# Performance work log

Hardware: AMD Instinct MI355X
Metric: run time of the kernel (lower is better)

## Reference

```python
import math
import jax, jax.numpy as jnp
import numpy as np

D_MODEL = 1024
N_HEAD = 16
D_HEAD = 64
Q_LEN = 2048
MEM_LEN = 2048
K_LEN = MEM_LEN + Q_LEN
B = 1
LN_EPS = 1e-5


def setup_inputs() -> dict:
    key = jax.random.key(0)
    ks = jax.random.split(key, 8)
    hidden = jax.random.normal(ks[0], (B, Q_LEN, D_MODEL), dtype=jnp.float32)
    position_embedding = jax.random.normal(ks[1], (K_LEN, D_MODEL), dtype=jnp.float32)
    u = jax.random.normal(ks[2], (N_HEAD, D_HEAD), dtype=jnp.float32) * 0.02
    v = jax.random.normal(ks[3], (N_HEAD, D_HEAD), dtype=jnp.float32) * 0.02
    memory = jax.random.normal(ks[4], (B, MEM_LEN, D_MODEL), dtype=jnp.float32)
    # TXL causal mask: query i may attend to key j iff j <= i + MEM_LEN
    i = jnp.arange(Q_LEN)[:, None]
    j = jnp.arange(K_LEN)[None, :]
    mask = (j > (i + MEM_LEN))[None, None]  # (1,1,Q,K) bool, True = masked
    # weights (torch Linear has no bias here); stored as (in, out)
    s = 1.0 / math.sqrt(D_MODEL)
    W_qkv = jax.random.normal(ks[5], (D_MODEL, 3 * N_HEAD * D_HEAD), dtype=jnp.float32) * s
    W_pe = jax.random.normal(ks[6], (D_MODEL, N_HEAD * D_HEAD), dtype=jnp.float32) * s
    W_out = jax.random.normal(ks[7], (N_HEAD * D_HEAD, D_MODEL), dtype=jnp.float32) * (1.0 / math.sqrt(N_HEAD * D_HEAD))
    return {"hidden": hidden, "position_embedding": position_embedding, "u": u,
            "v": v, "mask": mask, "memory": memory,
            "W_qkv": W_qkv, "W_pe": W_pe, "W_out": W_out}


def _layer_norm(x):
    # elementwise_affine=False LayerNorm over last dim
    mu = jnp.mean(x, axis=-1, keepdims=True)
    var = jnp.var(x, axis=-1, keepdims=True)
    return (x - mu) / jnp.sqrt(var + LN_EPS)


def reference(hidden, position_embedding, u, v, mask, memory, W_qkv, W_pe, W_out):
    batch, q_len, _ = hidden.shape
    k_len = position_embedding.shape[0]
    scale = 1.0 / math.sqrt(D_HEAD)

    mh = jnp.concatenate([memory, hidden], axis=1)          # (B, k_len, d_model)
    qkv = mh @ W_qkv                                        # post-norm: no LN on input
    Q, K, V = jnp.split(qkv, 3, axis=-1)
    Q = Q[:, -q_len:, :]
    pe = position_embedding @ W_pe                          # (k_len, H*D)

    Q = Q.reshape(batch, q_len, N_HEAD, D_HEAD)
    K = K.reshape(batch, k_len, N_HEAD, D_HEAD)
    V = V.reshape(batch, k_len, N_HEAD, D_HEAD)
    pe = pe.reshape(batch, k_len, N_HEAD, D_HEAD)

    AC = jnp.einsum('bqhd,bkhd->bhqk', Q + u, K)
    BD = jnp.einsum('bqhd,bkhd->bhqk', Q + v, pe)
    # NOTE: the original module calls relative_shift(BD) but DISCARDS the
    # result, so BD is used unshifted. We faithfully reproduce that.
    score = (AC + BD) * scale
    score = jnp.where(mask, -jnp.inf, score)
    prob = jax.nn.softmax(score, axis=-1)                   # (B,H,Q,K)
    av = jnp.einsum('bhqk,bkhd->bqhd', prob, V)
    av = av.reshape(batch, q_len, N_HEAD * D_HEAD)
    attn_out = av @ W_out
    return _layer_norm(hidden + attn_out)                   # post-norm residual
```

## Files before the change

kernel.cpp:

```cpp
#include <hip/hip_runtime.h>

typedef __attribute__((ext_vector_type(4))) float f32x4;
typedef __attribute__((ext_vector_type(16))) float f32x16;
typedef __attribute__((ext_vector_type(8))) short bf16x8;
typedef __attribute__((ext_vector_type(4))) unsigned short u16x4;
typedef unsigned short u16;

#define DM 1024
#define NHEAD 16
#define DHEAD 64
#define QLEN 2048
#define MLEN 2048
#define KLEN 4096
#define QSCALE 0.18033688011112042f

__device__ __forceinline__ float bf2f(u16 u) {
    unsigned i = ((unsigned)u) << 16; float f; __builtin_memcpy(&f, &i, 4); return f;
}
__device__ __forceinline__ u16 f2bf(float f) {
    unsigned i; __builtin_memcpy(&i, &f, 4);
    unsigned r = i + 0x7fffu + ((i >> 16) & 1u);
    return (u16)(r >> 16);
}
__device__ __forceinline__ float exp2_fast(float x) {
#if __has_builtin(__builtin_amdgcn_exp2f)
    return __builtin_amdgcn_exp2f(x);
#else
    return exp2f(x);
#endif
}
__device__ __forceinline__ unsigned cvtpk_bf16(float lo, float hi) {
    unsigned r;
    asm("v_cvt_pk_bf16_f32 %0, %1, %2" : "=v"(r) : "v"(lo), "v"(hi));
    return r;
}
__device__ __forceinline__ void gl2lds16(const void* g, void* l) {
    __builtin_amdgcn_global_load_lds((const __attribute__((address_space(1))) void*)g,
                                     (__attribute__((address_space(3))) void*)l, 16, 0, 0);
}

__global__ __launch_bounds__(256) void prep(
    const float* __restrict__ memory, const float* __restrict__ hidden,
    const float* __restrict__ pos, const float* __restrict__ Wqkv,
    const float* __restrict__ Wpe, const float* __restrict__ Wout,
    u16* __restrict__ MH, u16* __restrict__ PEA,
    u16* __restrict__ WQKVT, u16* __restrict__ WPET, u16* __restrict__ WOUTT)
{
    __shared__ float ls[64][65];
    const int b = blockIdx.x, t = threadIdx.x;
    if (b < 8192) {
        size_t e = ((size_t)b * 256 + t) * 4;
        const size_t HALF = (size_t)KLEN * DM;
        f32x4 v; u16* dst;
        if (e < HALF) {
            size_t row = e >> 10, col = e & 1023;
            const float* src = (row < MLEN) ? (memory + row * DM) : (hidden + (row - MLEN) * DM);
            v = *(const f32x4*)(src + col);
            dst = MH + e;
        } else {
            size_t e2 = e - HALF;
            v = *(const f32x4*)(pos + e2);
            dst = PEA + e2;
        }
        u16x4 o;
        #pragma unroll
        for (int c = 0; c < 4; ++c) o[c] = f2bf(v[c]);
        *(u16x4*)dst = o;
        return;
    }
    int tb = b - 8192;
    const float* src; u16* dst; int N, bx, by;
    if (tb < 768)       { src = Wqkv; dst = WQKVT; N = 3 * DM; bx = tb % 48; by = tb / 48; }
    else if (tb < 1024) { int i = tb - 768;  src = Wpe;  dst = WPET;  N = DM; bx = i & 15; by = i >> 4; }
    else                { int i = tb - 1024; src = Wout; dst = WOUTT; N = DM; bx = i & 15; by = i >> 4; }
    const int n0 = bx * 64, k0 = by * 64;
    const int c = t & 63, rg = t >> 6;
    #pragma unroll
    for (int p = 0; p < 16; ++p) {
        int r = p * 4 + rg;
        ls[r][c] = src[(size_t)(k0 + r) * N + n0 + c];
    }
    __syncthreads();
    #pragma unroll
    for (int p = 0; p < 16; ++p) {
        int r = p * 4 + rg;
        dst[(size_t)(n0 + r) * DM + k0 + c] = f2bf(ls[c][r]);
    }
}

__global__ __launch_bounds__(256, 3) void gemm_qkvpe(
    const u16* __restrict__ MH, const u16* __restrict__ PEA,
    const u16* __restrict__ WQKVT, const u16* __restrict__ WPET,
    const float* __restrict__ u, const float* __restrict__ vv,
    u16* __restrict__ QHAT, u16* __restrict__ KHAT, u16* __restrict__ VB)
{
    __shared__ u16 lsA[128 * 64];
    __shared__ u16 lsB[128 * 64];
    const int b = blockIdx.x;
    int row0, col0, region; const u16 *A, *B;
    if (b < 512)      { row0 = (b >> 4) * 128; col0 = 1024 + (b & 15) * 128; A = MH; B = WQKVT;
                        region = (col0 < 2048) ? 1 : 2; }
    else if (b < 640) { int i = b - 512; row0 = 2048 + (i >> 3) * 128; col0 = (i & 7) * 128;
                        A = MH; B = WQKVT; region = 0; }
    else              { int i = b - 640; row0 = (i >> 3) * 128; col0 = (i & 7) * 128;
                        A = PEA; B = WPET; region = 3; }
    const int tid = threadIdx.x, wave = tid >> 6, lane = tid & 63;
    const int blk = lane >> 4, ln = lane & 15;
    const int wr = (wave >> 1) << 6, wc = (wave & 1) << 6;
    const int rstage = lane >> 3;
    const int cstage = (lane & 7) * 8;

    f32x4 acc[4][4];
    #pragma unroll
    for (int i = 0; i < 4; ++i)
        #pragma unroll
        for (int j = 0; j < 4; ++j) acc[i][j] = f32x4{0.f, 0.f, 0.f, 0.f};

    for (int k0 = 0; k0 < DM; k0 += 64) {
        #pragma unroll
        for (int t = 0; t < 4; ++t) {
            int chunk = wave * 4 + t;
            int r = chunk * 8 + rstage;
            gl2lds16(A + (size_t)(row0 + r) * DM + k0 + cstage, lsA + chunk * 512);
            gl2lds16(B + (size_t)(col0 + r) * DM + k0 + cstage, lsB + chunk * 512);
        }
        __syncthreads();
        #pragma unroll
        for (int kk = 0; kk < 2; ++kk) {
            bf16x8 af[4], bfr[4];
            #pragma unroll
            for (int i = 0; i < 4; ++i)
                af[i] = *(const bf16x8*)(lsA + (wr + i * 16 + ln) * 64 + kk * 32 + blk * 8);
            #pragma unroll
            for (int j = 0; j < 4; ++j)
                bfr[j] = *(const bf16x8*)(lsB + (wc + j * 16 + ln) * 64 + kk * 32 + blk * 8);
            #pragma unroll
            for (int i = 0; i < 4; ++i)
                #pragma unroll
                for (int j = 0; j < 4; ++j)
                    acc[i][j] = __builtin_amdgcn_mfma_f32_16x16x32_bf16(af[i], bfr[j], acc[i][j], 0, 0, 0);
        }
        __syncthreads();
    }
    #pragma unroll
    for (int i = 0; i < 4; ++i)
        #pragma unroll
        for (int j = 0; j < 4; ++j)
            #pragma unroll
            for (int r = 0; r < 4; ++r) {
                int row = row0 + wr + i * 16 + blk * 4 + r;
                int col = col0 + wc + j * 16 + ln;
                float val = acc[i][j][r];
                if (region == 0) {
                    int q = row - MLEN, h = col >> 6;
                    size_t base = ((size_t)h * QLEN + q) * 128 + (col & 63);
                    QHAT[base]      = f2bf((val + u[col]) * QSCALE);
                    QHAT[base + 64] = f2bf((val + vv[col]) * QSCALE);
                } else if (region == 1) {
                    int c = col - 1024, h = c >> 6;
                    KHAT[((size_t)h * KLEN + row) * 128 + (c & 63)] = f2bf(val);
                } else if (region == 2) {
                    VB[(size_t)row * DM + (col - 2048)] = f2bf(val);
                } else {
                    int h = col >> 6;
                    KHAT[((size_t)h * KLEN + row) * 128 + 64 + (col & 63)] = f2bf(val);
                }
            }
}

__global__ __launch_bounds__(256) void pack_vt(const u16* __restrict__ VB, u16* __restrict__ VT)
{
    __shared__ float ls[64][65];
    const int kt = blockIdx.x, h = blockIdx.y;
    const int t = threadIdx.x, c = t & 63, rg = t >> 6;
    #pragma unroll
    for (int p = 0; p < 16; ++p) {
        int r = p * 4 + rg;
        ls[r][c] = bf2f(VB[(size_t)(kt * 64 + r) * DM + h * 64 + c]);
    }
    __syncthreads();
    #pragma unroll
    for (int p = 0; p < 16; ++p) {
        int d = p * 4 + rg;
        VT[((size_t)h * DHEAD + d) * KLEN + kt * 64 + c] = f2bf(ls[c][d]);
    }
}

__global__ __launch_bounds__(256, 4) void attn_fused(
    const u16* __restrict__ QHAT, const u16* __restrict__ KHAT,
    const u16* __restrict__ VT, u16* __restrict__ OPb, float* __restrict__ ML)
{
    __shared__ __align__(16) u16 smem[18432];
    const int b = blockIdx.x;
    const int h  = ((b & 7) << 1) | ((b >> 3) & 1);
    const int ks = b >> 8;
    const int qb = (((b >> 4) & 15) + 4 * ks) & 15;
    const int tid = threadIdx.x;
    const int wave = tid >> 6, lane = tid & 63;
    const int l31 = lane & 31, hi = lane >> 5;
    const int qrow0 = qb * 128 + wave * 32;
    u16* pb = smem + 13312 + wave * 1280;
    const int px = (l31 >> 3) & 3;

    const u16* khp = KHAT + (size_t)h * KLEN * 128;
    const u16* vhp = VT + (size_t)h * DHEAD * KLEN;

    const int nt = qb + 17;
    const int kbase = ks * nt * 32;
    const int vd = tid >> 2, vc = tid & 3;
    const int vslot = vc ^ ((vd >> 3) & 3);

    auto stage_load = [&](int buf, int kt) -> bf16x8 {
        const int k0 = kbase + kt * 32;
        u16* Kb = smem + buf * 4096;
        #pragma unroll
        for (int i = 0; i < 2; ++i) {
            int c = i * 256 + tid;
            int row = c >> 4, cgl = c & 15;
            int cs = cgl ^ (row & 15);
            gl2lds16(khp + ((size_t)(k0 + row) << 7) + cs * 8,
                     Kb + (size_t)(i * 256 + (tid & ~63)) * 8);
        }
        return *(const bf16x8*)(vhp + (size_t)vd * KLEN + k0 + vc * 8);
    };
    auto stage_write = [&](int buf, bf16x8 vr) {
        *(bf16x8*)(smem + 8192 + buf * 2560 + vd * 40 + vslot * 8) = vr;
    };

    bf16x8 qf[8];
    {
        const u16* qbase = QHAT + ((size_t)h * QLEN + qrow0 + l31) * 128 + hi * 8;
        #pragma unroll
        for (int kd = 0; kd < 8; ++kd) qf[kd] = *(const bf16x8*)(qbase + kd * 16);
    }

    f32x16 oacc[2];
    #pragma unroll
    for (int dg = 0; dg < 2; ++dg)
        #pragma unroll
        for (int r = 0; r < 16; ++r) oacc[dg][r] = 0.f;
    float mi = -1e30f, li = 0.f;

    const int qlim = qrow0 + 31 + MLEN;
    const int qsel = qrow0 + l31 + MLEN;

    bf16x8 vreg = stage_load(0, 0);
    asm volatile("s_waitcnt vmcnt(0)" ::: "memory");
    stage_write(0, vreg);
    __syncthreads();

    int cur = 0;
    for (int kt = 0; kt < nt; ++kt) {
        const int k0 = kbase + kt * 32;
        const bool pre = (kt + 1 < nt);
        if (pre) vreg = stage_load(cur ^ 1, kt + 1);

        if (k0 <= qlim) {
            f32x16 sacc;
            #pragma unroll
            for (int r = 0; r < 16; ++r) sacc[r] = 0.f;
            const u16* kb = smem + cur * 4096;
            const int rx = l31 & 15;
            #pragma unroll
            for (int kd = 0; kd < 8; ++kd) {
                int cd = (kd * 2 + hi) ^ rx;
                bf16x8 kf = *(const bf16x8*)(kb + l31 * 128 + cd * 8);
                sacc = __builtin_amdgcn_mfma_f32_32x32x16_bf16(kf, qf[kd], sacc, 0, 0, 0);
            }
            if (k0 + 31 > qrow0 + MLEN) {
                const int keyb = k0 + 4 * hi;
                #pragma unroll
                for (int r = 0; r < 16; ++r) {
                    int key = keyb + (r & 3) + 8 * (r >> 2);
                    if (key > qsel) sacc[r] = -1e30f;
                }
            }
            float mt;
            {
                f32x4 m4;
                #pragma unroll
                for (int r = 0; r < 4; ++r)
                    m4[r] = fmaxf(fmaxf(sacc[r], sacc[4 + r]), fmaxf(sacc[8 + r], sacc[12 + r]));
                mt = fmaxf(fmaxf(m4[0], m4[1]), fmaxf(m4[2], m4[3]));
            }
            mt = fmaxf(mt, __shfl_xor(mt, 32, 64));
            if (!__all(mt <= mi + 8.f)) {
                float mn = fmaxf(mi, mt);
                float corr = exp2_fast(mi - mn);
                mi = mn;
                li *= corr;
                #pragma unroll
                for (int dg = 0; dg < 2; ++dg)
                    #pragma unroll
                    for (int r = 0; r < 16; ++r) oacc[dg][r] *= corr;
            }
            #pragma unroll
            for (int r = 0; r < 16; ++r) sacc[r] = exp2_fast(sacc[r] - mi);
            float rs;
            {
                f32x4 s4;
                #pragma unroll
                for (int r = 0; r < 4; ++r)
                    s4[r] = (sacc[r] + sacc[4 + r]) + (sacc[8 + r] + sacc[12 + r]);
                rs = (s4[0] + s4[1]) + (s4[2] + s4[3]);
            }
            li += rs + __shfl_xor(rs, 32, 64);
            {
                unsigned* pd = (unsigned*)(pb + (size_t)l31 * 40);
                #pragma unroll
                for (int b2 = 0; b2 < 4; ++b2)
                    #pragma unroll
                    for (int c = 0; c < 2; ++c)
                        pd[(b2 ^ px) * 4 + 2 * hi + c] =
                            cvtpk_bf16(sacc[4 * b2 + 2 * c], sacc[4 * b2 + 2 * c + 1]);
            }
            #pragma unroll
            for (int kkl = 0; kkl < 2; ++kkl) {
                bf16x8 pf = *(const bf16x8*)(pb + (size_t)l31 * 40 + ((kkl * 2 + hi) ^ px) * 8);
                #pragma unroll
                for (int dg = 0; dg < 2; ++dg) {
                    int vrow = dg * 32 + l31;
                    int cd = (kkl * 2 + hi) ^ ((l31 >> 3) & 3);
                    bf16x8 vf = *(const bf16x8*)(smem + 8192 + cur * 2560 + vrow * 40 + cd * 8);
                    oacc[dg] = __builtin_amdgcn_mfma_f32_32x32x16_bf16(vf, pf, oacc[dg], 0, 0, 0);
                }
            }
        }
        asm volatile("s_waitcnt vmcnt(0)" ::: "memory");
        if (pre) stage_write(cur ^ 1, vreg);
        __syncthreads();
        cur ^= 1;
    }

    const int q = qrow0 + l31;
    unsigned* op32 = (unsigned*)(OPb + (((size_t)ks * QLEN + q) * NHEAD + h) * 64);
    #pragma unroll
    for (int dg = 0; dg < 2; ++dg) {
        union { f32x16 v; float f[16]; } oo;
        oo.v = oacc[dg];
        #pragma unroll
        for (int b2 = 0; b2 < 4; ++b2)
            #pragma unroll
            for (int c = 0; c < 2; ++c)
                op32[(dg * 32 + 8 * b2 + 4 * hi) / 2 + c] =
                    cvtpk_bf16(oo.f[4 * b2 + 2 * c], oo.f[4 * b2 + 2 * c + 1]);
    }
    if (!hi) {
        float* ml = ML + (((size_t)ks * QLEN + q) * NHEAD + h) * 2;
        ml[0] = mi; ml[1] = li;
    }
}

__global__ __launch_bounds__(256) void attn_combine(
    const u16* __restrict__ OPb, const float* __restrict__ ML, u16* __restrict__ AVB)
{
    int idx = blockIdx.x * 256 + threadIdx.x;
    int d8 = (idx & 7) * 8;
    int h  = (idx >> 3) & 15;
    int q  = idx >> 7;
    float m[4], l[4], mf = -1e30f;
    #pragma unroll
    for (int ks = 0; ks < 4; ++ks) {
        const float* ml = ML + (((size_t)ks * QLEN + q) * NHEAD + h) * 2;
        m[ks] = ml[0]; l[ks] = ml[1];
        mf = fmaxf(mf, m[ks]);
    }
    float lsum = 0.f;
    float a[4];
    #pragma unroll
    for (int ks = 0; ks < 4; ++ks) {
        a[ks] = exp2_fast(m[ks] - mf);
        lsum += a[ks] * l[ks];
    }
    float inv = 1.f / lsum;
    float acc[8];
    #pragma unroll
    for (int j = 0; j < 8; ++j) acc[j] = 0.f;
    #pragma unroll
    for (int ks = 0; ks < 4; ++ks) {
        float w = a[ks] * inv;
        const u16* src = OPb + (((size_t)ks * QLEN + q) * NHEAD + h) * 64 + d8;
        u16x4 x0 = *(const u16x4*)(src);
        u16x4 x1 = *(const u16x4*)(src + 4);
        #pragma unroll
        for (int j = 0; j < 4; ++j) { acc[j] += w * bf2f(x0[j]); acc[4 + j] += w * bf2f(x1[j]); }
    }
    unsigned* A32 = (unsigned*)AVB;
    size_t base = ((size_t)q * DM + h * 64 + d8) >> 1;
    #pragma unroll
    for (int j = 0; j < 4; ++j)
        A32[base + j] = cvtpk_bf16(acc[2 * j], acc[2 * j + 1]);
}

__global__ __launch_bounds__(256, 3) void gemm_out(
    const u16* __restrict__ A, const u16* __restrict__ Bt, float* __restrict__ RES)
{
    __shared__ u16 lsA[128 * 64];
    __shared__ u16 lsB[128 * 64];
    const int b = blockIdx.x;
    const int tile = b >> 1, kh = b & 1;
    const int row0 = (tile >> 3) * 128, col0 = (tile & 7) * 128;
    const int tid = threadIdx.x, wave = tid >> 6, lane = tid & 63;
    const int blk = lane >> 4, ln = lane & 15;
    const int wr = (wave >> 1) << 6, wc = (wave & 1) << 6;
    const int rstage = lane >> 3;
    const int cstage = (lane & 7) * 8;

    f32x4 acc[4][4];
    #pragma unroll
    for (int i = 0; i < 4; ++i)
        #pragma unroll
        for (int j = 0; j < 4; ++j) acc[i][j] = f32x4{0.f, 0.f, 0.f, 0.f};

    for (int k0 = kh * 512; k0 < kh * 512 + 512; k0 += 64) {
        #pragma unroll
        for (int t = 0; t < 4; ++t) {
            int chunk = wave * 4 + t;
            int r = chunk * 8 + rstage;
            gl2lds16(A  + (size_t)(row0 + r) * DM + k0 + cstage, lsA + chunk * 512);
            gl2lds16(Bt + (size_t)(col0 + r) * DM + k0 + cstage, lsB + chunk * 512);
        }
        __syncthreads();
        #pragma unroll
        for (int kk = 0; kk < 2; ++kk) {
            bf16x8 af[4], bfr[4];
            #pragma unroll
            for (int i = 0; i < 4; ++i)
                af[i] = *(const bf16x8*)(lsA + (wr + i * 16 + ln) * 64 + kk * 32 + blk * 8);
            #pragma unroll
            for (int j = 0; j < 4; ++j)
                bfr[j] = *(const bf16x8*)(lsB + (wc + j * 16 + ln) * 64 + kk * 32 + blk * 8);
            #pragma unroll
            for (int i = 0; i < 4; ++i)
                #pragma unroll
                for (int j = 0; j < 4; ++j)
                    acc[i][j] = __builtin_amdgcn_mfma_f32_16x16x32_bf16(af[i], bfr[j], acc[i][j], 0, 0, 0);
        }
        __syncthreads();
    }
    float* C = RES + (size_t)kh * QLEN * DM;
    #pragma unroll
    for (int i = 0; i < 4; ++i)
        #pragma unroll
        for (int j = 0; j < 4; ++j)
            #pragma unroll
            for (int r = 0; r < 4; ++r) {
                int row = row0 + wr + i * 16 + blk * 4 + r;
                int col = col0 + wc + j * 16 + ln;
                C[(size_t)row * DM + col] = acc[i][j][r];
            }
}

__global__ __launch_bounds__(256) void ln_kernel(
    const float* __restrict__ hidden, const float* __restrict__ RES, float* __restrict__ out)
{
    const int row = blockIdx.x, t = threadIdx.x;
    const int wave = t >> 6, lane = t & 63;
    __shared__ float ws[8];
    f32x4 a = ((const f32x4*)(hidden + (size_t)row * DM))[t];
    f32x4 r0 = ((const f32x4*)(RES + (size_t)row * DM))[t];
    f32x4 r1 = ((const f32x4*)(RES + (size_t)(QLEN + row) * DM))[t];
    f32x4 v;
    #pragma unroll
    for (int c = 0; c < 4; ++c) v[c] = a[c] + r0[c] + r1[c];
    float s = v[0] + v[1] + v[2] + v[3];
    float s2 = v[0] * v[0] + v[1] * v[1] + v[2] * v[2] + v[3] * v[3];
    #pragma unroll
    for (int off = 1; off < 64; off <<= 1) {
        s += __shfl_xor(s, off, 64);
        s2 += __shfl_xor(s2, off, 64);
    }
    if (lane == 0) { ws[wave] = s; ws[4 + wave] = s2; }
    __syncthreads();
    float ts = ws[0] + ws[1] + ws[2] + ws[3];
    float ts2 = ws[4] + ws[5] + ws[6] + ws[7];
    float mu = ts * (1.f / DM);
    float var = ts2 * (1.f / DM) - mu * mu;
    float rsq = rsqrtf(var + 1e-5f);
    f32x4 o;
    #pragma unroll
    for (int c = 0; c < 4; ++c) o[c] = (v[c] - mu) * rsq;
    ((f32x4*)(out + (size_t)row * DM))[t] = o;
}

extern "C" void kernel_launch(void* const* d_in, const int* in_sizes, int n_in,
                              void* d_out, int out_size, void* d_ws, size_t ws_size,
                              hipStream_t stream)
{
    const float* hidden = (const float*)d_in[0];
    const float* pos    = (const float*)d_in[1];
    const float* u      = (const float*)d_in[2];
    const float* vv     = (const float*)d_in[3];
    const float* memory = (const float*)d_in[5];
    const float* Wqkv   = (const float*)d_in[6];
    const float* Wpe    = (const float*)d_in[7];
    const float* Wout   = (const float*)d_in[8];
    float* out = (float*)d_out;

    char* w = (char*)d_ws;
    auto alloc = [&](size_t bytes) {
        void* p = (void*)w;
        w += (bytes + 255) & ~(size_t)255;
        return p;
    };
    u16* MH    = (u16*)alloc((size_t)KLEN * DM * 2);
    u16* PEA   = (u16*)alloc((size_t)KLEN * DM * 2);
    u16* WQKVT = (u16*)alloc((size_t)3 * DM * DM * 2);
    u16* WPET  = (u16*)alloc((size_t)DM * DM * 2);
    u16* VB    = (u16*)alloc((size_t)KLEN * DM * 2);
    u16* QHAT  = (u16*)alloc((size_t)NHEAD * QLEN * 128 * 2);
    u16* KHAT  = (u16*)alloc((size_t)NHEAD * KLEN * 128 * 2);
    u16* VTb   = (u16*)alloc((size_t)NHEAD * DHEAD * KLEN * 2);
    u16* AVB   = (u16*)alloc((size_t)QLEN * DM * 2);
    float* RES = (float*)alloc((size_t)2 * QLEN * DM * 4);
    u16* WOUTT = (u16*)alloc((size_t)DM * DM * 2);
    u16* OPb   = (u16*)d_ws;
    float* ML  = (float*)((char*)d_ws + (size_t)4 * QLEN * NHEAD * 64 * 2);

    prep<<<8192 + 1280, 256, 0, stream>>>(memory, hidden, pos, Wqkv, Wpe, Wout,
                                          MH, PEA, WQKVT, WPET, WOUTT);
    gemm_qkvpe<<<896, 256, 0, stream>>>(MH, PEA, WQKVT, WPET, u, vv, QHAT, KHAT, VB);
    pack_vt<<<dim3(KLEN / 64, NHEAD), 256, 0, stream>>>(VB, VTb);
    attn_fused<<<dim3(1024), 256, 0, stream>>>(QHAT, KHAT, VTb, OPb, ML);
    attn_combine<<<dim3(QLEN * NHEAD * 8 / 256), 256, 0, stream>>>(OPb, ML, AVB);
    gemm_out<<<256, 256, 0, stream>>>(AVB, WOUTT, RES);
    ln_kernel<<<QLEN, 256, 0, stream>>>(hidden, RES, out);
}
```

Measured before the change: 160.0 us.

## Triple-buffer GEMM LDS staging with swizzled layout and block remap

Both projection GEMMs now use a three-slot LDS ring with a 32-wide K step, prefetching two stages ahead and using a partial vmcnt wait so global-to-LDS loads overlap MFMA work. A single barrier per step replaces the two barriers per step used before. LDS rows are XOR-swizzled to cut bank conflicts on fragment reads. The KV block index is remapped so neighbouring blocks share input row panels, which should improve L2 reuse. The vmcnt count and the clamped tail prefetch rely on exact ordering of the async loads, so a mismatch there could read stale data.

```diff
diff --git a/kernel.cpp b/kernel.cpp
--- a/kernel.cpp
+++ b/kernel.cpp
@@ -94,12 +94,16 @@
     const float* __restrict__ u, const float* __restrict__ vv,
     u16* __restrict__ QHAT, u16* __restrict__ KHAT, u16* __restrict__ VB)
 {
-    __shared__ u16 lsA[128 * 64];
-    __shared__ u16 lsB[128 * 64];
+    __shared__ __align__(16) u16 ls[3 * 2 * 128 * 32];
     const int b = blockIdx.x;
     int row0, col0, region; const u16 *A, *B;
-    if (b < 512)      { row0 = (b >> 4) * 128; col0 = 1024 + (b & 15) * 128; A = MH; B = WQKVT;
-                        region = (col0 < 2048) ? 1 : 2; }
+    if (b < 512) {
+        int x = b & 7, idx = b >> 3;
+        int rp = (x >> 1) * 8 + (idx >> 3);
+        int c  = (x & 1) * 8 + (idx & 7);
+        row0 = rp * 128; col0 = 1024 + c * 128;
+        A = MH; B = WQKVT; region = (c < 8) ? 1 : 2;
+    }
     else if (b < 640) { int i = b - 512; row0 = 2048 + (i >> 3) * 128; col0 = (i & 7) * 128;
                         A = MH; B = WQKVT; region = 0; }
     else              { int i = b - 640; row0 = (i >> 3) * 128; col0 = (i & 7) * 128;
@@ -107,8 +111,19 @@
     const int tid = threadIdx.x, wave = tid >> 6, lane = tid & 63;
     const int blk = lane >> 4, ln = lane & 15;
     const int wr = (wave >> 1) << 6, wc = (wave & 1) << 6;
-    const int rstage = lane >> 3;
-    const int cstage = (lane & 7) * 8;
+
+    auto stage = [&](int slot, int kt) {
+        const int k0 = kt * 32;
+        u16* base = ls + slot * (2 * 128 * 32);
+        #pragma unroll
+        for (int i = 0; i < 2; ++i) {
+            int c = i * 256 + tid;
+            int row = c >> 2, s = c & 3;
+            int col8 = (s ^ ((row >> 1) & 3)) * 8;
+            gl2lds16(A + (size_t)(row0 + row) * DM + k0 + col8, base + c * 8);
+            gl2lds16(B + (size_t)(col0 + row) * DM + k0 + col8, base + 128 * 32 + c * 8);
+        }
+    };
 
     f32x4 acc[4][4];
     #pragma unroll
@@ -116,32 +131,34 @@
         #pragma unroll
         for (int j = 0; j < 4; ++j) acc[i][j] = f32x4{0.f, 0.f, 0.f, 0.f};
 
-    for (int k0 = 0; k0 < DM; k0 += 64) {
-        #pragma unroll
-        for (int t = 0; t < 4; ++t) {
-            int chunk = wave * 4 + t;
-            int r = chunk * 8 + rstage;
-            gl2lds16(A + (size_t)(row0 + r) * DM + k0 + cstage, lsA + chunk * 512);
-            gl2lds16(B + (size_t)(col0 + r) * DM + k0 + cstage, lsB + chunk * 512);
-        }
+    stage(0, 0);
+    stage(1, 1);
+    const int NSTEP = DM / 32;
+    for (int t = 0; t < NSTEP; ++t) {
+        asm volatile("s_waitcnt vmcnt(4)" ::: "memory");
         __syncthreads();
-        #pragma unroll
-        for (int kk = 0; kk < 2; ++kk) {
-            bf16x8 af[4], bfr[4];
-            #pragma unroll
-            for (int i = 0; i < 4; ++i)
-                af[i] = *(const bf16x8*)(lsA + (wr + i * 16 + ln) * 64 + kk * 32 + blk * 8);
+        int kt2 = (t + 2 < NSTEP) ? t + 2 : NSTEP - 1;
+        stage((t + 2) % 3, kt2);
+        const u16* la = ls + (t % 3) * (2 * 128 * 32);
+        const u16* lb = la + 128 * 32;
+        bf16x8 af[4], bfr[4];
+        #pragma unroll
+        for (int i = 0; i < 4; ++i) {
+            int ro = wr + i * 16 + ln;
+            af[i] = *(const bf16x8*)(la + ro * 32 + ((blk ^ ((ro >> 1) & 3)) * 8));
+        }
+        #pragma unroll
+        for (int j = 0; j < 4; ++j) {
+            int ro = wc + j * 16 + ln;
+            bfr[j] = *(const bf16x8*)(lb + ro * 32 + ((blk ^ ((ro >> 1) & 3)) * 8));
+        }
+        #pragma unroll
+        for (int i = 0; i < 4; ++i)
             #pragma unroll
             for (int j = 0; j < 4; ++j)
-                bfr[j] = *(const bf16x8*)(lsB + (wc + j * 16 + ln) * 64 + kk * 32 + blk * 8);
-            #pragma unroll
-            for (int i = 0; i < 4; ++i)
-                #pragma unroll
-                for (int j = 0; j < 4; ++j)
-                    acc[i][j] = __builtin_amdgcn_mfma_f32_16x16x32_bf16(af[i], bfr[j], acc[i][j], 0, 0, 0);
-        }
-        __syncthreads();
-    }
+                acc[i][j] = __builtin_amdgcn_mfma_f32_16x16x32_bf16(af[i], bfr[j], acc[i][j], 0, 0, 0);
+    }
+
     #pragma unroll
     for (int i = 0; i < 4; ++i)
         #pragma unroll
@@ -395,16 +412,27 @@
 __global__ __launch_bounds__(256, 3) void gemm_out(
     const u16* __restrict__ A, const u16* __restrict__ Bt, float* __restrict__ RES)
 {
-    __shared__ u16 lsA[128 * 64];
-    __shared__ u16 lsB[128 * 64];
+    __shared__ __align__(16) u16 ls[3 * 2 * 128 * 32];
     const int b = blockIdx.x;
     const int tile = b >> 1, kh = b & 1;
     const int row0 = (tile >> 3) * 128, col0 = (tile & 7) * 128;
     const int tid = threadIdx.x, wave = tid >> 6, lane = tid & 63;
     const int blk = lane >> 4, ln = lane & 15;
     const int wr = (wave >> 1) << 6, wc = (wave & 1) << 6;
-    const int rstage = lane >> 3;
-    const int cstage = (lane & 7) * 8;
+    const int kbase = kh * 512;
+
+    auto stage = [&](int slot, int kt) {
+        const int k0 = kbase + kt * 32;
+        u16* base = ls + slot * (2 * 128 * 32);
+        #pragma unroll
+        for (int i = 0; i < 2; ++i) {
+            int c = i * 256 + tid;
+            int row = c >> 2, s = c & 3;
+            int col8 = (s ^ ((row >> 1) & 3)) * 8;
+            gl2lds16(A  + (size_t)(row0 + row) * DM + k0 + col8, base + c * 8);
+            gl2lds16(Bt + (size_t)(col0 + row) * DM + k0 + col8, base + 128 * 32 + c * 8);
+        }
+    };
 
     f32x4 acc[4][4];
     #pragma unroll
@@ -412,31 +440,32 @@
         #pragma unroll
         for (int j = 0; j < 4; ++j) acc[i][j] = f32x4{0.f, 0.f, 0.f, 0.f};
 
-    for (int k0 = kh * 512; k0 < kh * 512 + 512; k0 += 64) {
-        #pragma unroll
-        for (int t = 0; t < 4; ++t) {
-            int chunk = wave * 4 + t;
-            int r = chunk * 8 + rstage;
-            gl2lds16(A  + (size_t)(row0 + r) * DM + k0 + cstage, lsA + chunk * 512);
-            gl2lds16(Bt + (size_t)(col0 + r) * DM + k0 + cstage, lsB + chunk * 512);
-        }
+    stage(0, 0);
+    stage(1, 1);
+    const int NSTEP = 16;
+    for (int t = 0; t < NSTEP; ++t) {
+        asm volatile("s_waitcnt vmcnt(4)" ::: "memory");
         __syncthreads();
-        #pragma unroll
-        for (int kk = 0; kk < 2; ++kk) {
-            bf16x8 af[4], bfr[4];
-            #pragma unroll
-            for (int i = 0; i < 4; ++i)
-                af[i] = *(const bf16x8*)(lsA + (wr + i * 16 + ln) * 64 + kk * 32 + blk * 8);
+        int kt2 = (t + 2 < NSTEP) ? t + 2 : NSTEP - 1;
+        stage((t + 2) % 3, kt2);
+        const u16* la = ls + (t % 3) * (2 * 128 * 32);
+        const u16* lb = la + 128 * 32;
+        bf16x8 af[4], bfr[4];
+        #pragma unroll
+        for (int i = 0; i < 4; ++i) {
+            int ro = wr + i * 16 + ln;
+            af[i] = *(const bf16x8*)(la + ro * 32 + ((blk ^ ((ro >> 1) & 3)) * 8));
+        }
+        #pragma unroll
+        for (int j = 0; j < 4; ++j) {
+            int ro = wc + j * 16 + ln;
+            bfr[j] = *(const bf16x8*)(lb + ro * 32 + ((blk ^ ((ro >> 1) & 3)) * 8));
+        }
+        #pragma unroll
+        for (int i = 0; i < 4; ++i)
             #pragma unroll
             for (int j = 0; j < 4; ++j)
-                bfr[j] = *(const bf16x8*)(lsB + (wc + j * 16 + ln) * 64 + kk * 32 + blk * 8);
-            #pragma unroll
-            for (int i = 0; i < 4; ++i)
-                #pragma unroll
-                for (int j = 0; j < 4; ++j)
-                    acc[i][j] = __builtin_amdgcn_mfma_f32_16x16x32_bf16(af[i], bfr[j], acc[i][j], 0, 0, 0);
-        }
-        __syncthreads();
+                acc[i][j] = __builtin_amdgcn_mfma_f32_16x16x32_bf16(af[i], bfr[j], acc[i][j], 0, 0, 0);
     }
     float* C = RES + (size_t)kh * QLEN * DM;
     #pragma unroll
```

Result: slower. 163.5 us (+2.2%).
